# Performance work log

Hardware: AMD Instinct MI355X
Metric: run time of the kernel (lower is better)

The kernel has to match this reference:

```python
import jax, jax.numpy as jnp
import numpy as np


def setup_inputs() -> dict:
    key = jax.random.key(0)
    k1, k2, k3 = jax.random.split(key, 3)
    N_SRC, N_DST, E, D = 100000, 100000, 1600000, 64
    h = jax.random.normal(k1, (N_SRC, D), dtype=jnp.float32)
    src_idx = jax.random.randint(k2, (E,), 0, N_SRC, dtype=jnp.int32)
    dst_idx = jax.random.randint(k3, (E,), 0, N_DST, dtype=jnp.int32)
    return {"h": h, "src_idx": src_idx, "dst_idx": dst_idx,
            "num_src": N_SRC, "num_dst": N_DST}


def reference(h, src_idx, dst_idx, num_src, num_dst):
    # norm_2 = -1 (default)
    ones = jnp.ones(src_idx.shape[0], dtype=h.dtype)
    # out-degree of src nodes, in-degree of dst nodes (clamped to >= 1)
    out_deg = jnp.clip(jax.ops.segment_sum(ones, src_idx, num_segments=num_src), 1.0)
    in_deg = jnp.clip(jax.ops.segment_sum(ones, dst_idx, num_segments=num_dst), 1.0)
    norm_src = out_deg ** -1.0  # [N_src]
    norm_dst = in_deg ** -1.0   # [N_dst]
    # scale source features, gather per edge, scatter-sum into dst
    feat_src = h * norm_src[:, None]               # [N_src, D]
    msgs = feat_src[src_idx]                       # [E, D]
    rst = jax.ops.segment_sum(msgs, dst_idx, num_segments=num_dst)  # [N_dst, D]
    return rst * norm_dst[:, None]
```

## Files before the change

kernel.cpp:

```cpp
#include <hip/hip_runtime.h>

#define D 64
#define SCAN_B 256
#define NBUCK 256
#define BSH 9
#define BMSK 511
#define NCHUNK 256

typedef __attribute__((ext_vector_type(8))) unsigned short ushort8_t;

__device__ __forceinline__ unsigned short f2bf(float f) {
    unsigned u = __float_as_uint(f);
    unsigned r = (u + 0x7FFFu + ((u >> 16) & 1u)) >> 16;
    return (unsigned short)r;
}


__global__ void p1_count(const int* __restrict__ src, const int* __restrict__ dst, int E,
                         int epc, int* __restrict__ cnt) {
    __shared__ int cd[NBUCK], cs[NBUCK];
    int c = blockIdx.x;
    for (int i = threadIdx.x; i < NBUCK; i += blockDim.x) { cd[i] = 0; cs[i] = 0; }
    __syncthreads();
    int beg = c * epc, end = min(E, beg + epc);
    for (int i = beg + threadIdx.x; i < end; i += blockDim.x) {
        atomicAdd(&cd[((unsigned)dst[i]) >> BSH], 1);
        atomicAdd(&cs[((unsigned)src[i]) >> BSH], 1);
    }
    __syncthreads();
    for (int b = threadIdx.x; b < NBUCK; b += blockDim.x) {
        cnt[(size_t)b * NCHUNK + c] = cd[b];
        cnt[(size_t)(NBUCK + b) * NCHUNK + c] = cs[b];
    }
}

__global__ void scanA_kernel(int* __restrict__ cnt, int* __restrict__ btot) {
    __shared__ int lds[NCHUNK];
    int g = blockIdx.x;
    int* e = cnt + (size_t)g * NCHUNK;
    int t = threadIdx.x;
    int v = e[t];
    lds[t] = v;
    __syncthreads();
    for (int off = 1; off < NCHUNK; off <<= 1) {
        int add = (t >= off) ? lds[t - off] : 0;
        __syncthreads();
        lds[t] += add;
        __syncthreads();
    }
    int incl = lds[t];
    e[t] = incl - v;
    if (t == NCHUNK - 1) btot[g] = incl;
}

__global__ void scanB_kernel(int* __restrict__ btot) {
    __shared__ int lds[NBUCK];
    int t = threadIdx.x;
    int a0 = btot[2 * t], a1 = btot[2 * t + 1];
    int p = a0 + a1;
    lds[t] = p;
    __syncthreads();
    for (int off = 1; off < 256; off <<= 1) {
        int v = (t >= off) ? lds[t - off] : 0;
        __syncthreads();
        lds[t] += v;
        __syncthreads();
    }
    int incl = lds[t];
    int excl = incl - p;
    btot[2 * t] = excl;
    btot[2 * t + 1] = excl + a0;
}

__global__ void p2_scatter(const int* __restrict__ src, const int* __restrict__ dst, int E,
                           int epc, const int* __restrict__ cnt, const int* __restrict__ btot,
                           int* __restrict__ packD, unsigned short* __restrict__ srtS) {
    __shared__ int curD[NBUCK], curS[NBUCK];
    int c = blockIdx.x;
    for (int b = threadIdx.x; b < NBUCK; b += blockDim.x) {
        curD[b] = btot[b] + cnt[(size_t)b * NCHUNK + c];
        curS[b] = btot[NBUCK + b] + cnt[(size_t)(NBUCK + b) * NCHUNK + c] - E;
    }
    __syncthreads();
    int beg = c * epc, end = min(E, beg + epc);
    for (int i = beg + threadIdx.x; i < end; i += blockDim.x) {
        int d = dst[i], s = src[i];
        int pd = atomicAdd(&curD[((unsigned)d) >> BSH], 1);
        packD[pd] = (s << BSH) | (d & BMSK);
        int ps = atomicAdd(&curS[((unsigned)s) >> BSH], 1);
        srtS[ps] = (unsigned short)(s & BMSK);
    }
}

__global__ void p3_merged(const int* __restrict__ packD, const unsigned short* __restrict__ srtS,
                          const int* __restrict__ btot, const float4* __restrict__ h4,
                          int E, int n_dst, int n_src,
                          int* __restrict__ csr, int2* __restrict__ od_arr,
                          unsigned short* __restrict__ featb) {
    __shared__ int hist[512];
    __shared__ int scan_s[256];
    __shared__ float nrm[512];
    int blk = blockIdx.x;
    int t = threadIdx.x;
    if (blk < NBUCK) {
        int b = blk;
        int beg = btot[b];
        int end = btot[b + 1];
        hist[t] = 0; hist[t + 256] = 0;
        __syncthreads();
        for (int i = beg + t; i < end; i += 256)
            atomicAdd(&hist[packD[i] & BMSK], 1);
        __syncthreads();
        int a0 = hist[2 * t], a1 = hist[2 * t + 1];
        int p = a0 + a1;
        scan_s[t] = p;
        __syncthreads();
        for (int off = 1; off < 256; off <<= 1) {
            int v = (t >= off) ? scan_s[t - off] : 0;
            __syncthreads();
            scan_s[t] += v;
            __syncthreads();
        }
        int e0 = scan_s[t] - p;
        int dbin0 = b * 512 + 2 * t;
        int dbin1 = dbin0 + 1;
        if (dbin0 < n_dst) od_arr[dbin0] = make_int2(beg + e0, a0);
        if (dbin1 < n_dst) od_arr[dbin1] = make_int2(beg + e0 + a0, a1);
        hist[2 * t] = e0;
        hist[2 * t + 1] = e0 + a0;
        __syncthreads();
        for (int i = beg + t; i < end; i += 256) {
            int v = packD[i];
            int pos = beg + atomicAdd(&hist[v & BMSK], 1);
            csr[pos] = v >> BSH;
        }
    } else {
        int row = blk;
        int b = blk - NBUCK;
        int beg = btot[row] - E;
        int end = ((row + 1 < 2 * NBUCK) ? btot[row + 1] : 2 * E) - E;
        hist[t] = 0; hist[t + 256] = 0;
        __syncthreads();
        for (int i = beg + t; i < end; i += 256)
            atomicAdd(&hist[srtS[i]], 1);
        __syncthreads();
        {
            int h0 = hist[t];       if (h0 < 1) h0 = 1;
            int h1 = hist[t + 256]; if (h1 < 1) h1 = 1;
            nrm[t] = 1.0f / (float)h0;
            nrm[t + 256] = 1.0f / (float)h1;
        }
        __syncthreads();
        for (int i = t; i < 512 * 8; i += 256) {
            int r = i >> 3, l8 = i & 7;
            int gsrc = b * 512 + r;
            if (gsrc < n_src) {
                float nm = nrm[r];
                float4 v0 = h4[(size_t)gsrc * 16 + l8 * 2];
                float4 v1 = h4[(size_t)gsrc * 16 + l8 * 2 + 1];
                ushort8_t o;
                o[0] = f2bf(v0.x * nm); o[1] = f2bf(v0.y * nm);
                o[2] = f2bf(v0.z * nm); o[3] = f2bf(v0.w * nm);
                o[4] = f2bf(v1.x * nm); o[5] = f2bf(v1.y * nm);
                o[6] = f2bf(v1.z * nm); o[7] = f2bf(v1.w * nm);
                *(ushort8_t*)(featb + (size_t)gsrc * 64 + l8 * 8) = o;
            }
        }
    }
}

__global__ void gather_feat(const unsigned short* __restrict__ featb,
                            const int* __restrict__ csr,
                            const int2* __restrict__ od_arr,
                            float4* __restrict__ out4, int n_dst) {
    int gid = blockIdx.x * blockDim.x + threadIdx.x;
    int row = gid >> 6;
    if (row >= n_dst) return;
    int lane = threadIdx.x & 63;
    int g = lane >> 3;
    int l8 = lane & 7;
    int2 od = od_arr[row];
    int beg = od.x, dg = od.y;
    int end = beg + dg;
    float a[8] = {0.f, 0.f, 0.f, 0.f, 0.f, 0.f, 0.f, 0.f};
    for (int k = beg + g; k < end; k += 16) {
        int s0 = csr[k];
        ushort8_t v0 = *(const ushort8_t*)(featb + (size_t)s0 * 64 + l8 * 8);
        int k2 = k + 8;
        if (k2 < end) {
            int s1 = csr[k2];
            ushort8_t v1 = *(const ushort8_t*)(featb + (size_t)s1 * 64 + l8 * 8);
            #pragma unroll
            for (int j = 0; j < 8; ++j)
                a[j] += __uint_as_float(((unsigned)v0[j]) << 16)
                      + __uint_as_float(((unsigned)v1[j]) << 16);
        } else {
            #pragma unroll
            for (int j = 0; j < 8; ++j)
                a[j] += __uint_as_float(((unsigned)v0[j]) << 16);
        }
    }
    #pragma unroll
    for (int m = 8; m < 64; m <<= 1) {
        #pragma unroll
        for (int j = 0; j < 8; ++j) a[j] += __shfl_xor(a[j], m);
    }
    if (g == 0) {
        float nd = 1.0f / (float)(dg < 1 ? 1 : dg);
        float4 r0, r1;
        r0.x = a[0] * nd; r0.y = a[1] * nd; r0.z = a[2] * nd; r0.w = a[3] * nd;
        r1.x = a[4] * nd; r1.y = a[5] * nd; r1.z = a[6] * nd; r1.w = a[7] * nd;
        out4[(size_t)row * 16 + l8 * 2]     = r0;
        out4[(size_t)row * 16 + l8 * 2 + 1] = r1;
    }
}

__global__ void scan1_kernel(const int* __restrict__ deg, int n,
                             int* __restrict__ out, int* __restrict__ bsums) {
    __shared__ int tmp[SCAN_B];
    int t = blockIdx.x * SCAN_B + threadIdx.x;
    int v = (t < n) ? deg[t] : 0;
    tmp[threadIdx.x] = v;
    __syncthreads();
    for (int off = 1; off < SCAN_B; off <<= 1) {
        int add = (threadIdx.x >= off) ? tmp[threadIdx.x - off] : 0;
        __syncthreads();
        tmp[threadIdx.x] += add;
        __syncthreads();
    }
    if (t < n) out[t] = tmp[threadIdx.x] - v;
    if (threadIdx.x == SCAN_B - 1) bsums[blockIdx.x] = tmp[threadIdx.x];
}

__global__ void scan2_kernel(int* __restrict__ bsums, int nb) {
    __shared__ int tmp[1024];
    __shared__ int carry_s;
    if (threadIdx.x == 0) carry_s = 0;
    __syncthreads();
    for (int base = 0; base < nb; base += 1024) {
        int i = base + threadIdx.x;
        int v = (i < nb) ? bsums[i] : 0;
        tmp[threadIdx.x] = v;
        __syncthreads();
        for (int off = 1; off < 1024; off <<= 1) {
            int add = (threadIdx.x >= off) ? tmp[threadIdx.x - off] : 0;
            __syncthreads();
            tmp[threadIdx.x] += add;
            __syncthreads();
        }
        int incl = tmp[threadIdx.x];
        int carry = carry_s;
        if (i < nb) bsums[i] = incl - v + carry;
        __syncthreads();
        if (threadIdx.x == 0) carry_s = carry + tmp[1023];
        __syncthreads();
    }
}

__global__ void scan3_kernel(int* __restrict__ out, const int* __restrict__ bsums, int n) {
    int t = blockIdx.x * SCAN_B + threadIdx.x;
    if (t < n) out[t] += bsums[blockIdx.x];
}

__global__ void gather_kernel(const float4* __restrict__ h4, const int* __restrict__ csr_src,
                              const int* __restrict__ offset, const int* __restrict__ deg_dst,
                              const float* __restrict__ norm_src,
                              float4* __restrict__ out4, int n_dst) {
    int gid = blockIdx.x * blockDim.x + threadIdx.x;
    int row = gid >> 6;
    if (row >= n_dst) return;
    int lane = threadIdx.x & 63;
    int g = lane >> 4;
    int l16 = lane & 15;
    int beg = offset[row];
    int deg = deg_dst[row];
    int end = beg + deg;
    float ax = 0.f, ay = 0.f, az = 0.f, aw = 0.f;
    for (int k = beg + g; k < end; k += 4) {
        int s = csr_src[k];
        float ns = norm_src[s];
        float4 v = h4[s * 16 + l16];
        ax = fmaf(v.x, ns, ax);
        ay = fmaf(v.y, ns, ay);
        az = fmaf(v.z, ns, az);
        aw = fmaf(v.w, ns, aw);
    }
    ax += __shfl_xor(ax, 16); ay += __shfl_xor(ay, 16);
    az += __shfl_xor(az, 16); aw += __shfl_xor(aw, 16);
    ax += __shfl_xor(ax, 32); ay += __shfl_xor(ay, 32);
    az += __shfl_xor(az, 32); aw += __shfl_xor(aw, 32);
    if (g == 0) {
        int dg = deg < 1 ? 1 : deg;
        float nd = 1.0f / (float)dg;
        float4 r;
        r.x = ax * nd; r.y = ay * nd; r.z = az * nd; r.w = aw * nd;
        out4[row * 16 + l16] = r;
    }
}

__global__ void degree_kernel(const int* __restrict__ src, const int* __restrict__ dst,
                              int E, int* __restrict__ deg_src, int* __restrict__ deg_dst) {
    int t = blockIdx.x * blockDim.x + threadIdx.x;
    int base = t * 4;
    if (base + 3 < E) {
        int4 s = *(const int4*)(src + base);
        int4 d = *(const int4*)(dst + base);
        atomicAdd(&deg_src[s.x], 1); atomicAdd(&deg_src[s.y], 1);
        atomicAdd(&deg_src[s.z], 1); atomicAdd(&deg_src[s.w], 1);
        atomicAdd(&deg_dst[d.x], 1); atomicAdd(&deg_dst[d.y], 1);
        atomicAdd(&deg_dst[d.z], 1); atomicAdd(&deg_dst[d.w], 1);
    } else {
        for (int i = base; i < E; ++i) {
            atomicAdd(&deg_src[src[i]], 1);
            atomicAdd(&deg_dst[dst[i]], 1);
        }
    }
}

__global__ void norm_src_kernel(const int* __restrict__ deg_src, int n_src,
                                float* __restrict__ norm_src) {
    int t = blockIdx.x * blockDim.x + threadIdx.x;
    if (t < n_src) {
        int s = deg_src[t]; if (s < 1) s = 1;
        norm_src[t] = 1.0f / (float)s;
    }
}

__global__ void fill_kernel(const int* __restrict__ src, const int* __restrict__ dst, int E,
                            const int* __restrict__ offset, int* __restrict__ cursor,
                            int* __restrict__ csr_src) {
    int t = blockIdx.x * blockDim.x + threadIdx.x;
    int base = t * 4;
    if (base + 3 < E) {
        int4 s = *(const int4*)(src + base);
        int4 d = *(const int4*)(dst + base);
        int p;
        p = offset[d.x] + atomicAdd(&cursor[d.x], 1); csr_src[p] = s.x;
        p = offset[d.y] + atomicAdd(&cursor[d.y], 1); csr_src[p] = s.y;
        p = offset[d.z] + atomicAdd(&cursor[d.z], 1); csr_src[p] = s.z;
        p = offset[d.w] + atomicAdd(&cursor[d.w], 1); csr_src[p] = s.w;
    } else {
        for (int i = base; i < E; ++i) {
            int d = dst[i];
            int p = offset[d] + atomicAdd(&cursor[d], 1);
            csr_src[p] = src[i];
        }
    }
}

__global__ void scatter_kernel(const float* __restrict__ h,
                               const int* __restrict__ src, const int* __restrict__ dst,
                               const float* __restrict__ norm_src,
                               float* __restrict__ out, int E) {
    long long t = (long long)blockIdx.x * blockDim.x + threadIdx.x;
    int e = (int)(t >> 6);
    if (e >= E) return;
    int j = (int)(t & 63);
    int s = src[e];
    float v = h[s * D + j] * norm_src[s];
    unsafeAtomicAdd(&out[dst[e] * D + j], v);
}

__global__ void scale_kernel(float* __restrict__ out, const int* __restrict__ deg_dst, int n) {
    int t = blockIdx.x * blockDim.x + threadIdx.x;
    if (t < n) {
        int dg = deg_dst[t >> 6]; if (dg < 1) dg = 1;
        out[t] *= 1.0f / (float)dg;
    }
}

static inline size_t align16(size_t x) { return (x + 15) & ~(size_t)15; }

extern "C" void kernel_launch(void* const* d_in, const int* in_sizes, int n_in,
                              void* d_out, int out_size, void* d_ws, size_t ws_size,
                              hipStream_t stream) {
    const float* h   = (const float*)d_in[0];
    const int*   src = (const int*)d_in[1];
    const int*   dst = (const int*)d_in[2];
    float* out = (float*)d_out;

    const int E     = in_sizes[1];
    const int n_src = in_sizes[0] / D;
    const int n_dst = out_size / D;
    const int n_cnt = 2 * NBUCK * NCHUNK;
    const int epc = (E + NCHUNK - 1) / NCHUNK;

    char* w = (char*)d_ws;
    size_t off = 0;
    size_t o_cnt   = off; off = align16(off + (size_t)n_cnt * 4);
    size_t o_btot  = off; off = align16(off + (size_t)(2 * NBUCK) * 4);
    size_t o_packD = off; off = align16(off + (size_t)E * 4);
    size_t o_csr   = off; off = align16(off + (size_t)E * 4);
    size_t o_od    = off; off = align16(off + (size_t)n_dst * 8);
    size_t o_feat  = off; off = align16(off + (size_t)n_src * 64 * 2);
    size_t o_srtS  = off; off = align16(off + (size_t)E * 2);
    size_t needA = off;

    if (ws_size >= needA && n_src <= NBUCK * 512 && n_dst <= NBUCK * 512) {
        int* cnt    = (int*)(w + o_cnt);
        int* btot   = (int*)(w + o_btot);
        int* packD  = (int*)(w + o_packD);
        int* csr    = (int*)(w + o_csr);
        int2* od    = (int2*)(w + o_od);
        unsigned short* featb = (unsigned short*)(w + o_feat);
        unsigned short* srtS  = (unsigned short*)(w + o_srtS);

        p1_count<<<NCHUNK, 512, 0, stream>>>(src, dst, E, epc, cnt);
        scanA_kernel<<<2 * NBUCK, NCHUNK, 0, stream>>>(cnt, btot);
        scanB_kernel<<<1, 256, 0, stream>>>(btot);
        p2_scatter<<<NCHUNK, 512, 0, stream>>>(src, dst, E, epc, cnt, btot, packD, srtS);
        p3_merged<<<2 * NBUCK, 256, 0, stream>>>(packD, srtS, btot, (const float4*)h,
                                                 E, n_dst, n_src, csr, od, featb);
        long long gthreads = (long long)n_dst * D;
        gather_feat<<<(int)((gthreads + 255) / 256), 256, 0, stream>>>(
            featb, csr, od, (float4*)out, n_dst);
        return;
    }

    const int nbB = (n_dst + SCAN_B - 1) / SCAN_B;
    const int nbB_pad = ((nbB + 1023) / 1024) * 1024;
    const int eb4 = (E + 4 * 256 - 1) / (4 * 256);
    const int nblk = ((n_src > n_dst ? n_src : n_dst) + 255) / 256;
    size_t needB = ((size_t)n_src * 2 + (size_t)n_dst * 3 + nbB_pad) * 4 + (size_t)E * 4;

    if (ws_size >= needB) {
        int* deg_src = (int*)d_ws;
        int* deg_dst = deg_src + n_src;
        int* cursor  = deg_dst + n_dst;
        int* offset  = cursor + n_dst;
        int* bsums   = offset + n_dst;
        float* norm_src = (float*)(bsums + nbB_pad);
        int* csr_src = (int*)(norm_src + n_src);

        hipMemsetAsync(d_ws, 0, sizeof(int) * (size_t)(n_src + 2 * (size_t)n_dst), stream);
        degree_kernel<<<eb4, 256, 0, stream>>>(src, dst, E, deg_src, deg_dst);
        norm_src_kernel<<<nblk, 256, 0, stream>>>(deg_src, n_src, norm_src);
        scan1_kernel<<<nbB, SCAN_B, 0, stream>>>(deg_dst, n_dst, offset, bsums);
        scan2_kernel<<<1, 1024, 0, stream>>>(bsums, nbB);
        scan3_kernel<<<nbB, SCAN_B, 0, stream>>>(offset, bsums, n_dst);
        fill_kernel<<<eb4, 256, 0, stream>>>(src, dst, E, offset, cursor, csr_src);
        long long gthreads = (long long)n_dst * D;
        gather_kernel<<<(int)((gthreads + 255) / 256), 256, 0, stream>>>(
            (const float4*)h, csr_src, offset, deg_dst, norm_src, (float4*)out, n_dst);
        return;
    }

    {
        int* deg_src = (int*)d_ws;
        int* deg_dst = deg_src + n_src;
        float* norm_src = (float*)(deg_dst + n_dst);
        hipMemsetAsync(d_ws, 0, sizeof(int) * (size_t)(n_src + n_dst), stream);
        hipMemsetAsync(d_out, 0, sizeof(float) * (size_t)out_size, stream);
        degree_kernel<<<eb4, 256, 0, stream>>>(src, dst, E, deg_src, deg_dst);
        norm_src_kernel<<<nblk, 256, 0, stream>>>(deg_src, n_src, norm_src);
        long long total = (long long)E * D;
        scatter_kernel<<<(int)((total + 255) / 256), 256, 0, stream>>>(h, src, dst, norm_src, out, E);
        scale_kernel<<<(out_size + 255) / 256, 256, 0, stream>>>(out, deg_dst, out_size);
    }
}
```

Measured before the change: 104.0 us.

## Fold bucket-total scan into scatter kernel and simplify bf16 unpacking in gather

Removes the single-block scanB launch. Each p2_scatter block now redundantly scans the 512 bucket totals in LDS, and block 0 writes the scanned result to a new btotS buffer for p3_merged. This saves one kernel launch and its serialization on the stream, at the cost of a short redundant 512-element scan (nine barrier steps) in every scatter block. The gather loop also loads features as uint4 and converts bf16 pairs with shift and mask instead of per-element ushort extraction.

```diff
diff --git a/kernel.cpp b/kernel.cpp
--- a/kernel.cpp
+++ b/kernel.cpp
@@ -14,6 +14,7 @@
     unsigned r = (u + 0x7FFFu + ((u >> 16) & 1u)) >> 16;
     return (unsigned short)r;
 }
+__device__ __forceinline__ float uf(unsigned u) { return __uint_as_float(u); }
 
 
 __global__ void p1_count(const int* __restrict__ src, const int* __restrict__ dst, int E,
@@ -53,37 +54,35 @@
     if (t == NCHUNK - 1) btot[g] = incl;
 }
 
-__global__ void scanB_kernel(int* __restrict__ btot) {
-    __shared__ int lds[NBUCK];
-    int t = threadIdx.x;
-    int a0 = btot[2 * t], a1 = btot[2 * t + 1];
-    int p = a0 + a1;
-    lds[t] = p;
-    __syncthreads();
-    for (int off = 1; off < 256; off <<= 1) {
-        int v = (t >= off) ? lds[t - off] : 0;
-        __syncthreads();
-        lds[t] += v;
-        __syncthreads();
-    }
-    int incl = lds[t];
-    int excl = incl - p;
-    btot[2 * t] = excl;
-    btot[2 * t + 1] = excl + a0;
-}
-
 __global__ void p2_scatter(const int* __restrict__ src, const int* __restrict__ dst, int E,
                            int epc, const int* __restrict__ cnt, const int* __restrict__ btot,
+                           int* __restrict__ btotS,
                            int* __restrict__ packD, unsigned short* __restrict__ srtS) {
+    __shared__ int scn[2 * NBUCK];
     __shared__ int curD[NBUCK], curS[NBUCK];
     int c = blockIdx.x;
-    for (int b = threadIdx.x; b < NBUCK; b += blockDim.x) {
-        curD[b] = btot[b] + cnt[(size_t)b * NCHUNK + c];
-        curS[b] = btot[NBUCK + b] + cnt[(size_t)(NBUCK + b) * NCHUNK + c] - E;
+    int t = threadIdx.x;
+    int raw = btot[t];
+    scn[t] = raw;
+    __syncthreads();
+    for (int off = 1; off < 2 * NBUCK; off <<= 1) {
+        int v = (t >= off) ? scn[t - off] : 0;
+        __syncthreads();
+        scn[t] += v;
+        __syncthreads();
+    }
+    int excl = scn[t] - raw;
+    __syncthreads();
+    scn[t] = excl;
+    __syncthreads();
+    if (c == 0) btotS[t] = excl;
+    if (t < NBUCK) {
+        curD[t] = scn[t] + cnt[(size_t)t * NCHUNK + c];
+        curS[t] = scn[NBUCK + t] + cnt[(size_t)(NBUCK + t) * NCHUNK + c] - E;
     }
     __syncthreads();
     int beg = c * epc, end = min(E, beg + epc);
-    for (int i = beg + threadIdx.x; i < end; i += blockDim.x) {
+    for (int i = beg + t; i < end; i += blockDim.x) {
         int d = dst[i], s = src[i];
         int pd = atomicAdd(&curD[((unsigned)d) >> BSH], 1);
         packD[pd] = (s << BSH) | (d & BMSK);
@@ -185,19 +184,28 @@
     float a[8] = {0.f, 0.f, 0.f, 0.f, 0.f, 0.f, 0.f, 0.f};
     for (int k = beg + g; k < end; k += 16) {
         int s0 = csr[k];
-        ushort8_t v0 = *(const ushort8_t*)(featb + (size_t)s0 * 64 + l8 * 8);
+        uint4 v0 = *(const uint4*)(featb + (size_t)s0 * 64 + l8 * 8);
         int k2 = k + 8;
         if (k2 < end) {
             int s1 = csr[k2];
-            ushort8_t v1 = *(const ushort8_t*)(featb + (size_t)s1 * 64 + l8 * 8);
-            #pragma unroll
-            for (int j = 0; j < 8; ++j)
-                a[j] += __uint_as_float(((unsigned)v0[j]) << 16)
-                      + __uint_as_float(((unsigned)v1[j]) << 16);
+            uint4 v1 = *(const uint4*)(featb + (size_t)s1 * 64 + l8 * 8);
+            a[0] += uf(v0.x << 16) + uf(v1.x << 16);
+            a[1] += uf(v0.x & 0xFFFF0000u) + uf(v1.x & 0xFFFF0000u);
+            a[2] += uf(v0.y << 16) + uf(v1.y << 16);
+            a[3] += uf(v0.y & 0xFFFF0000u) + uf(v1.y & 0xFFFF0000u);
+            a[4] += uf(v0.z << 16) + uf(v1.z << 16);
+            a[5] += uf(v0.z & 0xFFFF0000u) + uf(v1.z & 0xFFFF0000u);
+            a[6] += uf(v0.w << 16) + uf(v1.w << 16);
+            a[7] += uf(v0.w & 0xFFFF0000u) + uf(v1.w & 0xFFFF0000u);
         } else {
-            #pragma unroll
-            for (int j = 0; j < 8; ++j)
-                a[j] += __uint_as_float(((unsigned)v0[j]) << 16);
+            a[0] += uf(v0.x << 16);
+            a[1] += uf(v0.x & 0xFFFF0000u);
+            a[2] += uf(v0.y << 16);
+            a[3] += uf(v0.y & 0xFFFF0000u);
+            a[4] += uf(v0.z << 16);
+            a[5] += uf(v0.z & 0xFFFF0000u);
+            a[6] += uf(v0.w << 16);
+            a[7] += uf(v0.w & 0xFFFF0000u);
         }
     }
     #pragma unroll
@@ -389,6 +397,7 @@
     size_t off = 0;
     size_t o_cnt   = off; off = align16(off + (size_t)n_cnt * 4);
     size_t o_btot  = off; off = align16(off + (size_t)(2 * NBUCK) * 4);
+    size_t o_btotS = off; off = align16(off + (size_t)(2 * NBUCK) * 4);
     size_t o_packD = off; off = align16(off + (size_t)E * 4);
     size_t o_csr   = off; off = align16(off + (size_t)E * 4);
     size_t o_od    = off; off = align16(off + (size_t)n_dst * 8);
@@ -399,6 +408,7 @@
     if (ws_size >= needA && n_src <= NBUCK * 512 && n_dst <= NBUCK * 512) {
         int* cnt    = (int*)(w + o_cnt);
         int* btot   = (int*)(w + o_btot);
+        int* btotS  = (int*)(w + o_btotS);
         int* packD  = (int*)(w + o_packD);
         int* csr    = (int*)(w + o_csr);
         int2* od    = (int2*)(w + o_od);
@@ -407,9 +417,9 @@
 
         p1_count<<<NCHUNK, 512, 0, stream>>>(src, dst, E, epc, cnt);
         scanA_kernel<<<2 * NBUCK, NCHUNK, 0, stream>>>(cnt, btot);
-        scanB_kernel<<<1, 256, 0, stream>>>(btot);
-        p2_scatter<<<NCHUNK, 512, 0, stream>>>(src, dst, E, epc, cnt, btot, packD, srtS);
-        p3_merged<<<2 * NBUCK, 256, 0, stream>>>(packD, srtS, btot, (const float4*)h,
+        p2_scatter<<<NCHUNK, 512, 0, stream>>>(src, dst, E, epc, cnt, btot, btotS,
+                                               packD, srtS);
+        p3_merged<<<2 * NBUCK, 256, 0, stream>>>(packD, srtS, btotS, (const float4*)h,
                                                  E, n_dst, n_src, csr, od, featb);
         long long gthreads = (long long)n_dst * D;
         gather_feat<<<(int)((gthreads + 255) / 256), 256, 0, stream>>>(
```

Result: no change. 103.4 us (-0.5%).
